# Kernel optimization log

Hardware: AMD Instinct MI355X
Metric: run time of the kernel (lower is better)

Reference implementation:

```python
import jax, jax.numpy as jnp
import numpy as np

TAU = 0.07          # softmax temperature
THR = 0.3           # Jaccard similarity threshold for positive pairs
EPS_NORM = 1e-12    # F.normalize eps


def setup_inputs() -> dict:
    key = jax.random.key(0)
    k1, k2, k3 = jax.random.split(key, 3)
    N, D, A = 4096, 128, 512
    z1 = jax.random.normal(k1, (N, D), dtype=jnp.float32)
    z2 = jax.random.normal(k2, (N, D), dtype=jnp.float32)
    labels = jax.random.randint(k3, (N, A), 0, 2).astype(jnp.int32)
    return {"z1": z1, "z2": z2, "labels": labels}


def _l2_normalize(x):
    n = jnp.linalg.norm(x, axis=-1, keepdims=True)
    return x / jnp.maximum(n, EPS_NORM)


def reference(z1, z2, labels):
    # Implements the N > 1000 (chunked) branch of SupConLoss.forward,
    # vectorized over all anchors at once (chunking is just tiling; math identical).
    N = z1.shape[0]
    idx = jnp.arange(N)

    z1n = _l2_normalize(z1)                       # (N, D)
    z2n = _l2_normalize(z2)                       # (N, D)
    z_all = jnp.concatenate([z1n, z2n], axis=0)   # (2N, D)

    # Jaccard label similarity -> positive-pair mask
    lab = labels.astype(jnp.float32)              # (N, A)
    inter = lab @ lab.T                           # (N, N)
    s = lab.sum(axis=1, keepdims=True)            # (N, 1)
    union = s + s.T - inter
    jaccard = inter / (union + 1e-8)
    pos_label = jaccard >= THR                    # (N, N) bool

    # pos mask over 2N columns: label-positives in both halves,
    # augmented view [j, N+j] forced True, self column [j, j] forced False.
    pos_mask = jnp.concatenate([pos_label, pos_label], axis=1)  # (N, 2N)
    pos_mask = pos_mask.at[idx, N + idx].set(True)
    pos_mask = pos_mask.at[idx, idx].set(False)

    # similarity of z1 anchors against all 2N embeddings
    sim = (z1n @ z_all.T) / TAU                   # (N, 2N)
    sim = sim - jax.lax.stop_gradient(sim.max(axis=1, keepdims=True))
    exp_sim = jnp.exp(sim)

    # denominator excludes the self column [j, j]
    denom = exp_sim.sum(axis=1, keepdims=True) - exp_sim[idx, idx][:, None]
    log_prob = sim - jnp.log(denom + 1e-8)

    num_pos = jnp.maximum(pos_mask.sum(axis=1), 1)
    loss_per_sample = -jnp.where(pos_mask, log_prob, 0.0).sum(axis=1) / num_pos
    return loss_per_sample.sum() / N
```

## Files before the change

### kernel.cpp

```cpp
#include <hip/hip_runtime.h>
#include <math.h>

#define N_ROWS 4096
#define DIM    128
#define A_LAB  512
#define INV_TAU 14.285714285714286f
#define C_EXP   20.609929155556620f

typedef __attribute__((ext_vector_type(8))) short short8;
typedef __attribute__((ext_vector_type(4))) float f32x4;
typedef __attribute__((ext_vector_type(4))) int i32x4;
typedef __attribute__((ext_vector_type(16))) int i32x16;


__device__ __forceinline__ unsigned short f2bf(float f) {
  unsigned int u = __builtin_bit_cast(unsigned int, f);
  u += 0x7fffu + ((u >> 16) & 1u);
  return (unsigned short)(u >> 16);
}

__device__ __forceinline__ void gl_lds16(const void* g, void* l) {
  __builtin_amdgcn_global_load_lds(
      (const __attribute__((address_space(1))) unsigned int*)g,
      (__attribute__((address_space(3))) unsigned int*)l, 16, 0, 0);
}

__global__ __launch_bounds__(256) void k_norm_pack(
    const float* __restrict__ z1, const float* __restrict__ z2,
    const int* __restrict__ labels,
    unsigned int* __restrict__ zbf, uint2* __restrict__ labs8,
    int* __restrict__ s, float* __restrict__ part, float* __restrict__ out)
{
  {
    const int idx = blockIdx.x * 256 + threadIdx.x;
    if (idx < 3 * 4096) part[idx] = 0.0f;
    if (idx == 0) out[0] = 0.0f;
  }
  const int wave = threadIdx.x >> 6, lane = threadIdx.x & 63;
  const int r = blockIdx.x * 4 + wave;
  const float* src = (r < N_ROWS) ? (z1 + (size_t)r * DIM)
                                  : (z2 + (size_t)(r - N_ROWS) * DIM);
  float2 x = ((const float2*)src)[lane];
  float ss = x.x * x.x + x.y * x.y;
  #pragma unroll
  for (int off = 32; off > 0; off >>= 1) ss += __shfl_xor(ss, off);
  const float inv = 1.0f / fmaxf(sqrtf(ss), 1e-12f);
  const unsigned int lo = f2bf(x.x * inv);
  const unsigned int hi = f2bf(x.y * inv);
  {
    const int U  = lane >> 2;
    const int Up = U ^ (r & 15);
    zbf[(size_t)r * 64 + Up * 4 + (lane & 3)] = (hi << 16) | lo;
  }

  if (r < N_ROWS) {
    const int4* lp = (const int4*)(labels + (size_t)r * A_LAB);
    const int4 a = lp[2 * lane], b = lp[2 * lane + 1];
    const unsigned int w0 = (unsigned int)(a.x != 0)       | ((unsigned int)(a.y != 0) << 8)
                          | ((unsigned int)(a.z != 0) << 16) | ((unsigned int)(a.w != 0) << 24);
    const unsigned int w1 = (unsigned int)(b.x != 0)       | ((unsigned int)(b.y != 0) << 8)
                          | ((unsigned int)(b.z != 0) << 16) | ((unsigned int)(b.w != 0) << 24);
    uint2 v; v.x = w0; v.y = w1;
    const int Ul  = lane >> 1;
    const int cc  = Ul >> 3, uu = Ul & 7;
    const int Ulp = (cc << 3) | (uu ^ (r & 7));
    labs8[(size_t)r * 64 + Ulp * 2 + (lane & 1)] = v;
    int cnt = __popc(w0) + __popc(w1);
    #pragma unroll
    for (int off = 32; off > 0; off >>= 1) cnt += __shfl_xor(cnt, off);
    if (lane == 0) s[r] = cnt;
  }
}

__global__ __launch_bounds__(256, 3) void k_fused(
    const unsigned char* __restrict__ labs8, const int* __restrict__ s,
    const unsigned short* __restrict__ zbf, float* __restrict__ part)
{
  __shared__ uint4 lds[2048];
  __shared__ unsigned int pmL[128 * 4];
  const int tid = threadIdx.x;
  const int ibase = blockIdx.x * 128, jbase = blockIdx.y * 128;
  const int wave = tid >> 6, lane = tid & 63;
  const bool diag = (ibase == jbase);

  const int jwr = (wave >> 1) * 64, jwc = (wave & 1) * 64;
  const int col32 = lane & 31, h = lane >> 5;

  const int s3i = 3 * s[ibase + jwr + lane];
  const int s3j = 3 * s[jbase + jwc + lane];

  i32x16 jacc[2][2];
  #pragma unroll
  for (int rt = 0; rt < 2; ++rt)
    #pragma unroll
    for (int nt = 0; nt < 2; ++nt)
      #pragma unroll
      for (int e = 0; e < 16; ++e) jacc[rt][nt][e] = 0;

  for (int ck = 0; ck < 4; ++ck) {
    if (ck) __syncthreads();
    #pragma unroll
    for (int it = 0; it < 4; ++it) {
      const int g = wave * 256 + it * 64 + lane;
      const int r = g >> 3, u = g & 7;
      const size_t go = (size_t)ck * 128 + u * 16;
      gl_lds16(labs8 + (((size_t)(ibase + r)) << 9) + go,
               &lds[wave * 256 + it * 64]);
      gl_lds16(labs8 + (((size_t)(jbase + r)) << 9) + go,
               &lds[1024 + wave * 256 + it * 64]);
    }
    __syncthreads();
    #pragma unroll
    for (int ks = 0; ks < 4; ++ks) {
      const int u = ks * 2 + h;
      i32x4 a[2], b[2];
      #pragma unroll
      for (int rt = 0; rt < 2; ++rt) {
        const int m = jwr + rt * 32 + col32;
        a[rt] = *(const i32x4*)&lds[m * 8 + (u ^ (m & 7))];
      }
      #pragma unroll
      for (int nt = 0; nt < 2; ++nt) {
        const int m = jwc + nt * 32 + col32;
        b[nt] = *(const i32x4*)&lds[1024 + m * 8 + (u ^ (m & 7))];
      }
      #pragma unroll
      for (int rt = 0; rt < 2; ++rt)
        #pragma unroll
        for (int nt = 0; nt < 2; ++nt)
          jacc[rt][nt] = __builtin_amdgcn_mfma_i32_32x32x32_i8(a[rt], b[nt], jacc[rt][nt], 0, 0, 0);
    }
  }

  __syncthreads();

  {
    const char* gz = (const char*)zbf;
    #pragma unroll
    for (int it = 0; it < 8; ++it) {
      const int g = wave * 512 + it * 64 + lane;
      const int r = g >> 4, u = g & 15;
      gl_lds16(gz + (size_t)(jbase + r) * 256 + u * 16, &lds[wave * 512 + it * 64]);
    }
  }

  const int col = lane & 15, quad = lane >> 4;
  const int swr = wave * 32;
  short8 afr[2][4];
  {
    const char* gz = (const char*)zbf;
    #pragma unroll
    for (int rt = 0; rt < 2; ++rt)
      #pragma unroll
      for (int kf = 0; kf < 4; ++kf) {
        const int ra = ibase + swr + rt * 16 + col;
        const int slot = (kf * 4 + quad) ^ (ra & 15);
        afr[rt][kf] = *(const short8*)(gz + (size_t)ra * 256 + slot * 16);
      }
  }

  #pragma unroll
  for (int rt = 0; rt < 2; ++rt)
    #pragma unroll
    for (int nt = 0; nt < 2; ++nt) {
      const int wl = (jwc >> 5) + nt;
      const int sj = __shfl(s3j, nt * 32 + col32);
      #pragma unroll
      for (int reg = 0; reg < 16; ++reg) {
        const int r0 = (reg & 3) + 8 * (reg >> 2);
        const int si = __shfl(s3i, rt * 32 + r0 + 4 * h);
        const bool pred = 13 * jacc[rt][nt][reg] >= si + sj;
        const unsigned long long bal = __ballot(pred);
        const int lr = jwr + rt * 32 + r0;
        if (lane == 0)      pmL[lr * 4 + wl]       = (unsigned int)bal;
        else if (lane == 1) pmL[(lr + 4) * 4 + wl] = (unsigned int)(bal >> 32);
      }
    }

  __syncthreads();

  float lacc[2][4], Sacc[2][4], Pcnt[2][4];
  #pragma unroll
  for (int rt = 0; rt < 2; ++rt)
    #pragma unroll
    for (int reg = 0; reg < 4; ++reg) { lacc[rt][reg] = 0; Sacc[rt][reg] = 0; Pcnt[rt][reg] = 0; }

  #pragma unroll
  for (int half = 0; half < 2; ++half) {
    f32x4 acc[2][8];
    #pragma unroll
    for (int rt = 0; rt < 2; ++rt)
      #pragma unroll
      for (int nt = 0; nt < 8; ++nt) acc[rt][nt] = (f32x4){0, 0, 0, 0};

    #pragma unroll
    for (int nt = 0; nt < 8; ++nt) {
      short8 bfr[4];
      #pragma unroll
      for (int kf = 0; kf < 4; ++kf) {
        const int r = nt * 16 + col;
        const int u = kf * 4 + quad;
        bfr[kf] = *(const short8*)&lds[r * 16 + (u ^ (r & 15))];
      }
      #pragma unroll
      for (int rt = 0; rt < 2; ++rt)
        #pragma unroll
        for (int kf = 0; kf < 4; ++kf)
          acc[rt][nt] = __builtin_amdgcn_mfma_f32_16x16x32_bf16(
              afr[rt][kf], bfr[kf], acc[rt][nt], 0, 0, 0);
    }

    if (half == 0) {
      __syncthreads();
      const char* gz = (const char*)zbf;
      #pragma unroll
      for (int it = 0; it < 8; ++it) {
        const int g = wave * 512 + it * 64 + lane;
        const int r = g >> 4, u = g & 15;
        gl_lds16(gz + (size_t)(N_ROWS + jbase + r) * 256 + u * 16,
                 &lds[wave * 512 + it * 64]);
      }
    }

    if (!diag) {
      #pragma unroll
      for (int rt = 0; rt < 2; ++rt) {
        unsigned int pw[4][4];
        #pragma unroll
        for (int reg = 0; reg < 4; ++reg) {
          const int li = swr + rt * 16 + quad * 4 + reg;
          #pragma unroll
          for (int w = 0; w < 4; ++w) pw[reg][w] = pmL[li * 4 + w];
        }
        #pragma unroll
        for (int nt = 0; nt < 8; ++nt) {
          const int joff = nt * 16 + col;
          const int bitpos = joff & 31;
          const int w = nt >> 1;
          #pragma unroll
          for (int reg = 0; reg < 4; ++reg) {
            const float d = acc[rt][nt][reg];
            const bool bit = (pw[reg][w] >> bitpos) & 1;
            lacc[rt][reg] += exp2f(fmaf(d, C_EXP, -C_EXP));
            if (bit) { Sacc[rt][reg] += d; Pcnt[rt][reg] += 1.0f; }
          }
        }
      }
    } else {
      const bool left = (half == 0);
      #pragma unroll
      for (int rt = 0; rt < 2; ++rt) {
        unsigned int pw[4][4];
        #pragma unroll
        for (int reg = 0; reg < 4; ++reg) {
          const int li = swr + rt * 16 + quad * 4 + reg;
          #pragma unroll
          for (int w = 0; w < 4; ++w) pw[reg][w] = pmL[li * 4 + w];
        }
        #pragma unroll
        for (int nt = 0; nt < 8; ++nt) {
          const int joff = nt * 16 + col;
          const int jc = jbase + joff;
          const int bitpos = joff & 31;
          const int w = nt >> 1;
          #pragma unroll
          for (int reg = 0; reg < 4; ++reg) {
            const int i = ibase + swr + rt * 16 + quad * 4 + reg;
            const float d = acc[rt][nt][reg];
            const bool bit = (pw[reg][w] >> bitpos) & 1;
            const bool self = left && (jc == i);
            const bool pos = left ? (bit && !self) : (bit || (jc == i));
            const float e = exp2f(fmaf(d, C_EXP, -C_EXP));
            if (!self) lacc[rt][reg] += e;
            if (pos) { Sacc[rt][reg] += d; Pcnt[rt][reg] += 1.0f; }
          }
        }
      }
    }
    if (half == 0) __syncthreads();
  }

  #pragma unroll
  for (int rt = 0; rt < 2; ++rt)
    #pragma unroll
    for (int reg = 0; reg < 4; ++reg) {
      float l = lacc[rt][reg], S = Sacc[rt][reg], P = Pcnt[rt][reg];
      #pragma unroll
      for (int m = 1; m < 16; m <<= 1) {
        l += __shfl_xor(l, m);
        S += __shfl_xor(S, m);
        P += __shfl_xor(P, m);
      }
      if (col == 0) {
        const int i = ibase + swr + rt * 16 + quad * 4 + reg;
        atomicAdd(&part[i], l);
        atomicAdd(&part[4096 + i], S);
        atomicAdd(&part[8192 + i], P);
      }
    }
}

__global__ __launch_bounds__(128) void k_loss(
    const float* __restrict__ part, float* __restrict__ out)
{
  const int a = blockIdx.x * 128 + threadIdx.x;
  const float l = part[a];
  const float S = part[4096 + a];
  const float P = part[8192 + a];
  const float np = fmaxf(P, 1.0f);
  float v = INV_TAU + logf(l + 1e-8f) - (S * INV_TAU) / np;
  #pragma unroll
  for (int off = 32; off > 0; off >>= 1) v += __shfl_xor(v, off);
  __shared__ float ws2[2];
  const int wave = threadIdx.x >> 6, lane = threadIdx.x & 63;
  if (lane == 0) ws2[wave] = v;
  __syncthreads();
  if (threadIdx.x == 0) atomicAdd(out, (ws2[0] + ws2[1]) * (1.0f / (float)N_ROWS));
}

extern "C" void kernel_launch(void* const* d_in, const int* in_sizes, int n_in,
                              void* d_out, int out_size, void* d_ws, size_t ws_size,
                              hipStream_t stream) {
  const float* z1 = (const float*)d_in[0];
  const float* z2 = (const float*)d_in[1];
  const int* labels = (const int*)d_in[2];
  float* out = (float*)d_out;
  char* ws = (char*)d_ws;

  unsigned int* zbf    = (unsigned int*)(ws);
  uint2* labs8         = (uint2*)(ws + 2097152);
  int* s               = (int*)(ws + 4194304);
  float* part          = (float*)(ws + 4210688);

  hipLaunchKernelGGL(k_norm_pack, dim3(2048), dim3(256), 0, stream,
                     z1, z2, labels, zbf, labs8, s, part, out);
  hipLaunchKernelGGL(k_fused, dim3(32, 32), dim3(256), 0, stream,
                     (const unsigned char*)labs8, s, (const unsigned short*)zbf, part);
  hipLaunchKernelGGL(k_loss, dim3(32), dim3(128), 0, stream, part, out);
}
```

Measured before the change: 109.4 us.

## Drop LDS staging, load MFMA operands directly from global/L2

Removes the LDS staging buffers and global_load_lds copies for label bytes and bf16 embeddings. MFMA operands are now read straight from global memory, which relies on L2/L1 reuse, and the XOR swizzle in the packing kernel is removed to match. Both halves of the similarity are computed before the epilogue, so off-diagonal tiles fuse their exp/sum work, and the positive count comes from popcounts of the mask instead of per-element counting. The change cuts barriers and LDS traffic but adds redundant global loads and more live accumulator registers; occupancy is lowered to 2 blocks per SIMD.

```diff
diff --git a/kernel.cpp b/kernel.cpp
--- a/kernel.cpp
+++ b/kernel.cpp
@@ -17,12 +17,6 @@
   unsigned int u = __builtin_bit_cast(unsigned int, f);
   u += 0x7fffu + ((u >> 16) & 1u);
   return (unsigned short)(u >> 16);
-}
-
-__device__ __forceinline__ void gl_lds16(const void* g, void* l) {
-  __builtin_amdgcn_global_load_lds(
-      (const __attribute__((address_space(1))) unsigned int*)g,
-      (__attribute__((address_space(3))) unsigned int*)l, 16, 0, 0);
 }
 
 __global__ __launch_bounds__(256) void k_norm_pack(
@@ -47,11 +41,7 @@
   const float inv = 1.0f / fmaxf(sqrtf(ss), 1e-12f);
   const unsigned int lo = f2bf(x.x * inv);
   const unsigned int hi = f2bf(x.y * inv);
-  {
-    const int U  = lane >> 2;
-    const int Up = U ^ (r & 15);
-    zbf[(size_t)r * 64 + Up * 4 + (lane & 3)] = (hi << 16) | lo;
-  }
+  zbf[(size_t)r * 64 + lane] = (hi << 16) | lo;
 
   if (r < N_ROWS) {
     const int4* lp = (const int4*)(labels + (size_t)r * A_LAB);
@@ -61,10 +51,7 @@
     const unsigned int w1 = (unsigned int)(b.x != 0)       | ((unsigned int)(b.y != 0) << 8)
                           | ((unsigned int)(b.z != 0) << 16) | ((unsigned int)(b.w != 0) << 24);
     uint2 v; v.x = w0; v.y = w1;
-    const int Ul  = lane >> 1;
-    const int cc  = Ul >> 3, uu = Ul & 7;
-    const int Ulp = (cc << 3) | (uu ^ (r & 7));
-    labs8[(size_t)r * 64 + Ulp * 2 + (lane & 1)] = v;
+    labs8[(size_t)r * 64 + lane] = v;
     int cnt = __popc(w0) + __popc(w1);
     #pragma unroll
     for (int off = 32; off > 0; off >>= 1) cnt += __shfl_xor(cnt, off);
@@ -72,16 +59,17 @@
   }
 }
 
-__global__ __launch_bounds__(256, 3) void k_fused(
+__global__ __launch_bounds__(256, 2) void k_fused(
     const unsigned char* __restrict__ labs8, const int* __restrict__ s,
     const unsigned short* __restrict__ zbf, float* __restrict__ part)
 {
-  __shared__ uint4 lds[2048];
   __shared__ unsigned int pmL[128 * 4];
   const int tid = threadIdx.x;
   const int ibase = blockIdx.x * 128, jbase = blockIdx.y * 128;
   const int wave = tid >> 6, lane = tid & 63;
   const bool diag = (ibase == jbase);
+  const char* gl = (const char*)labs8;
+  const char* gz = (const char*)zbf;
 
   const int jwr = (wave >> 1) * 64, jwc = (wave & 1) * 64;
   const int col32 = lane & 31, h = lane >> 5;
@@ -97,66 +85,26 @@
       #pragma unroll
       for (int e = 0; e < 16; ++e) jacc[rt][nt][e] = 0;
 
+  const int ra0 = ibase + jwr + col32;
+  const int rb0 = jbase + jwc + col32;
+  #pragma unroll
   for (int ck = 0; ck < 4; ++ck) {
-    if (ck) __syncthreads();
-    #pragma unroll
-    for (int it = 0; it < 4; ++it) {
-      const int g = wave * 256 + it * 64 + lane;
-      const int r = g >> 3, u = g & 7;
-      const size_t go = (size_t)ck * 128 + u * 16;
-      gl_lds16(labs8 + (((size_t)(ibase + r)) << 9) + go,
-               &lds[wave * 256 + it * 64]);
-      gl_lds16(labs8 + (((size_t)(jbase + r)) << 9) + go,
-               &lds[1024 + wave * 256 + it * 64]);
-    }
-    __syncthreads();
     #pragma unroll
     for (int ks = 0; ks < 4; ++ks) {
-      const int u = ks * 2 + h;
+      const int off = ck * 128 + ks * 32 + h * 16;
       i32x4 a[2], b[2];
       #pragma unroll
-      for (int rt = 0; rt < 2; ++rt) {
-        const int m = jwr + rt * 32 + col32;
-        a[rt] = *(const i32x4*)&lds[m * 8 + (u ^ (m & 7))];
-      }
-      #pragma unroll
-      for (int nt = 0; nt < 2; ++nt) {
-        const int m = jwc + nt * 32 + col32;
-        b[nt] = *(const i32x4*)&lds[1024 + m * 8 + (u ^ (m & 7))];
-      }
+      for (int rt = 0; rt < 2; ++rt)
+        a[rt] = *(const i32x4*)(gl + (size_t)(ra0 + rt * 32) * 512 + off);
+      #pragma unroll
+      for (int nt = 0; nt < 2; ++nt)
+        b[nt] = *(const i32x4*)(gl + (size_t)(rb0 + nt * 32) * 512 + off);
       #pragma unroll
       for (int rt = 0; rt < 2; ++rt)
         #pragma unroll
         for (int nt = 0; nt < 2; ++nt)
           jacc[rt][nt] = __builtin_amdgcn_mfma_i32_32x32x32_i8(a[rt], b[nt], jacc[rt][nt], 0, 0, 0);
     }
-  }
-
-  __syncthreads();
-
-  {
-    const char* gz = (const char*)zbf;
-    #pragma unroll
-    for (int it = 0; it < 8; ++it) {
-      const int g = wave * 512 + it * 64 + lane;
-      const int r = g >> 4, u = g & 15;
-      gl_lds16(gz + (size_t)(jbase + r) * 256 + u * 16, &lds[wave * 512 + it * 64]);
-    }
-  }
-
-  const int col = lane & 15, quad = lane >> 4;
-  const int swr = wave * 32;
-  short8 afr[2][4];
-  {
-    const char* gz = (const char*)zbf;
-    #pragma unroll
-    for (int rt = 0; rt < 2; ++rt)
-      #pragma unroll
-      for (int kf = 0; kf < 4; ++kf) {
-        const int ra = ibase + swr + rt * 16 + col;
-        const int slot = (kf * 4 + quad) ^ (ra & 15);
-        afr[rt][kf] = *(const short8*)(gz + (size_t)ra * 256 + slot * 16);
-      }
   }
 
   #pragma unroll
@@ -177,97 +125,96 @@
       }
     }
 
-  __syncthreads();
-
-  float lacc[2][4], Sacc[2][4], Pcnt[2][4];
-  #pragma unroll
-  for (int rt = 0; rt < 2; ++rt)
-    #pragma unroll
-    for (int reg = 0; reg < 4; ++reg) { lacc[rt][reg] = 0; Sacc[rt][reg] = 0; Pcnt[rt][reg] = 0; }
+  const int col = lane & 15, quad = lane >> 4;
+  const int swr = wave * 32;
+
+  short8 afr[2][4];
+  #pragma unroll
+  for (int rt = 0; rt < 2; ++rt)
+    #pragma unroll
+    for (int kf = 0; kf < 4; ++kf) {
+      const int ra = ibase + swr + rt * 16 + col;
+      afr[rt][kf] = *(const short8*)(gz + (size_t)ra * 256 + kf * 64 + quad * 16);
+    }
+
+  f32x4 acc[2][2][8];
+  #pragma unroll
+  for (int half = 0; half < 2; ++half)
+    #pragma unroll
+    for (int rt = 0; rt < 2; ++rt)
+      #pragma unroll
+      for (int nt = 0; nt < 8; ++nt) acc[half][rt][nt] = (f32x4){0, 0, 0, 0};
 
   #pragma unroll
   for (int half = 0; half < 2; ++half) {
-    f32x4 acc[2][8];
-    #pragma unroll
-    for (int rt = 0; rt < 2; ++rt)
-      #pragma unroll
-      for (int nt = 0; nt < 8; ++nt) acc[rt][nt] = (f32x4){0, 0, 0, 0};
-
+    const int cb = (half ? N_ROWS : 0) + jbase;
     #pragma unroll
     for (int nt = 0; nt < 8; ++nt) {
       short8 bfr[4];
       #pragma unroll
       for (int kf = 0; kf < 4; ++kf) {
-        const int r = nt * 16 + col;
-        const int u = kf * 4 + quad;
-        bfr[kf] = *(const short8*)&lds[r * 16 + (u ^ (r & 15))];
+        const int rb = cb + nt * 16 + col;
+        bfr[kf] = *(const short8*)(gz + (size_t)rb * 256 + kf * 64 + quad * 16);
       }
       #pragma unroll
       for (int rt = 0; rt < 2; ++rt)
         #pragma unroll
         for (int kf = 0; kf < 4; ++kf)
-          acc[rt][nt] = __builtin_amdgcn_mfma_f32_16x16x32_bf16(
-              afr[rt][kf], bfr[kf], acc[rt][nt], 0, 0, 0);
-    }
-
-    if (half == 0) {
-      __syncthreads();
-      const char* gz = (const char*)zbf;
-      #pragma unroll
-      for (int it = 0; it < 8; ++it) {
-        const int g = wave * 512 + it * 64 + lane;
-        const int r = g >> 4, u = g & 15;
-        gl_lds16(gz + (size_t)(N_ROWS + jbase + r) * 256 + u * 16,
-                 &lds[wave * 512 + it * 64]);
-      }
-    }
-
-    if (!diag) {
+          acc[half][rt][nt] = __builtin_amdgcn_mfma_f32_16x16x32_bf16(
+              afr[rt][kf], bfr[kf], acc[half][rt][nt], 0, 0, 0);
+    }
+  }
+
+  __syncthreads();
+
+  float lacc[2][4], Sacc[2][4], Pcnt[2][4];
+  #pragma unroll
+  for (int rt = 0; rt < 2; ++rt)
+    #pragma unroll
+    for (int reg = 0; reg < 4; ++reg) { lacc[rt][reg] = 0; Sacc[rt][reg] = 0; Pcnt[rt][reg] = 0; }
+
+  if (!diag) {
+    #pragma unroll
+    for (int rt = 0; rt < 2; ++rt) {
+      uint4 pw[4];
+      #pragma unroll
+      for (int reg = 0; reg < 4; ++reg)
+        pw[reg] = *(const uint4*)&pmL[(swr + rt * 16 + quad * 4 + reg) * 4];
+      #pragma unroll
+      for (int nt = 0; nt < 8; ++nt) {
+        const int bitpos = (nt & 1) * 16 + col;
+        #pragma unroll
+        for (int reg = 0; reg < 4; ++reg) {
+          const unsigned int w = ((const unsigned int*)&pw[reg])[nt >> 1];
+          const float d0 = acc[0][rt][nt][reg];
+          const float d1 = acc[1][rt][nt][reg];
+          lacc[rt][reg] += exp2f(fmaf(d0, C_EXP, -C_EXP))
+                         + exp2f(fmaf(d1, C_EXP, -C_EXP));
+          if ((w >> bitpos) & 1) Sacc[rt][reg] += d0 + d1;
+        }
+      }
+    }
+  } else {
+    #pragma unroll
+    for (int half = 0; half < 2; ++half) {
+      const bool left = (half == 0);
       #pragma unroll
       for (int rt = 0; rt < 2; ++rt) {
-        unsigned int pw[4][4];
-        #pragma unroll
-        for (int reg = 0; reg < 4; ++reg) {
-          const int li = swr + rt * 16 + quad * 4 + reg;
-          #pragma unroll
-          for (int w = 0; w < 4; ++w) pw[reg][w] = pmL[li * 4 + w];
-        }
-        #pragma unroll
-        for (int nt = 0; nt < 8; ++nt) {
-          const int joff = nt * 16 + col;
-          const int bitpos = joff & 31;
-          const int w = nt >> 1;
-          #pragma unroll
-          for (int reg = 0; reg < 4; ++reg) {
-            const float d = acc[rt][nt][reg];
-            const bool bit = (pw[reg][w] >> bitpos) & 1;
-            lacc[rt][reg] += exp2f(fmaf(d, C_EXP, -C_EXP));
-            if (bit) { Sacc[rt][reg] += d; Pcnt[rt][reg] += 1.0f; }
-          }
-        }
-      }
-    } else {
-      const bool left = (half == 0);
-      #pragma unroll
-      for (int rt = 0; rt < 2; ++rt) {
-        unsigned int pw[4][4];
-        #pragma unroll
-        for (int reg = 0; reg < 4; ++reg) {
-          const int li = swr + rt * 16 + quad * 4 + reg;
-          #pragma unroll
-          for (int w = 0; w < 4; ++w) pw[reg][w] = pmL[li * 4 + w];
-        }
+        uint4 pw[4];
+        #pragma unroll
+        for (int reg = 0; reg < 4; ++reg)
+          pw[reg] = *(const uint4*)&pmL[(swr + rt * 16 + quad * 4 + reg) * 4];
         #pragma unroll
         for (int nt = 0; nt < 8; ++nt) {
           const int joff = nt * 16 + col;
           const int jc = jbase + joff;
           const int bitpos = joff & 31;
-          const int w = nt >> 1;
           #pragma unroll
           for (int reg = 0; reg < 4; ++reg) {
             const int i = ibase + swr + rt * 16 + quad * 4 + reg;
-            const float d = acc[rt][nt][reg];
-            const bool bit = (pw[reg][w] >> bitpos) & 1;
+            const unsigned int w = ((const unsigned int*)&pw[reg])[nt >> 1];
+            const float d = acc[half][rt][nt][reg];
+            const bool bit = (w >> bitpos) & 1;
             const bool self = left && (jc == i);
             const bool pos = left ? (bit && !self) : (bit || (jc == i));
             const float e = exp2f(fmaf(d, C_EXP, -C_EXP));
@@ -277,7 +224,6 @@
         }
       }
     }
-    if (half == 0) __syncthreads();
   }
 
   #pragma unroll
@@ -289,10 +235,15 @@
       for (int m = 1; m < 16; m <<= 1) {
         l += __shfl_xor(l, m);
         S += __shfl_xor(S, m);
-        P += __shfl_xor(P, m);
+        if (diag) P += __shfl_xor(P, m);
       }
       if (col == 0) {
-        const int i = ibase + swr + rt * 16 + quad * 4 + reg;
+        const int li = swr + rt * 16 + quad * 4 + reg;
+        const int i = ibase + li;
+        if (!diag) {
+          const uint4 pw = *(const uint4*)&pmL[li * 4];
+          P = 2.0f * (float)(__popc(pw.x) + __popc(pw.y) + __popc(pw.z) + __popc(pw.w));
+        }
         atomicAdd(&part[i], l);
         atomicAdd(&part[4096 + i], S);
         atomicAdd(&part[8192 + i], P);
```

Result: slower. 151.7 us (+38.7%).
